# Performance work log

Hardware: AMD Instinct MI355X
Metric: run time of the kernel (lower is better)

## Reference

```python
import jax, jax.numpy as jnp
import numpy as np

C_ENC = 64
H_FEAT = 96
W_FEAT = 96
B = 2
Q = 32768
HID = 256
IN_DIM = C_ENC * 9 + 2 + 2  # 580
EPS_SHIFT = 1e-6


def _unfold3x3(feat):
    # F.unfold(feat, 3, padding=1).view(B, C*9, H, W)
    Bf, C, H, W = feat.shape
    p = jnp.pad(feat, ((0, 0), (0, 0), (1, 1), (1, 1)))
    shifts = [p[:, :, ki:ki + H, kj:kj + W] for ki in range(3) for kj in range(3)]
    return jnp.stack(shifts, axis=2).reshape(Bf, C * 9, H, W)


def _nearest_idx(g, size):
    # torch grid_sample nearest, align_corners=False: unnormalize then nearbyint
    ix = ((g + 1.0) * size - 1.0) * 0.5
    return jnp.clip(jnp.round(ix).astype(jnp.int32), 0, size - 1)


def _mlp(x, W0, b0, W1, b1, W2, b2, W3, b3, W4, b4):
    h = jax.nn.relu(x @ W0 + b0)
    h = jax.nn.relu(h @ W1 + b1)
    h = jax.nn.relu(h @ W2 + b2)
    h = jax.nn.relu(h @ W3 + b3)
    return h @ W4 + b4


def setup_inputs() -> dict:
    key = jax.random.key(0)
    ks = jax.random.split(key, 8)
    feat = jax.random.normal(ks[0], (B, C_ENC, H_FEAT, W_FEAT), jnp.float32)
    coord = jax.random.uniform(ks[1], (B, Q, 2), jnp.float32, -1.0, 1.0)
    # cell size for a ~181x181 HR grid: 2/181
    cell = jnp.full((B, Q, 2), 2.0 / 181.0, jnp.float32)
    s0 = 1.0 / np.sqrt(IN_DIM)
    sh = 1.0 / np.sqrt(HID)
    W0 = jax.random.normal(ks[2], (IN_DIM, HID), jnp.float32) * s0
    W1 = jax.random.normal(ks[3], (HID, HID), jnp.float32) * sh
    W2 = jax.random.normal(ks[4], (HID, HID), jnp.float32) * sh
    W3 = jax.random.normal(ks[5], (HID, HID), jnp.float32) * sh
    W4 = jax.random.normal(ks[6], (HID, 1), jnp.float32) * sh
    z = lambda n: jnp.zeros((n,), jnp.float32)
    return {"feat": feat, "coord": coord, "cell": cell,
            "W0": W0, "b0": z(HID), "W1": W1, "b1": z(HID),
            "W2": W2, "b2": z(HID), "W3": W3, "b3": z(HID),
            "W4": W4, "b4": z(1)}


def reference(feat, coord, cell, W0, b0, W1, b1, W2, b2, W3, b3, W4, b4):
    Bf, C, H, W = feat.shape
    feat_u = _unfold3x3(feat)                     # (B, C*9, H, W)
    feat_flat = feat_u.reshape(Bf, C * 9, H * W)  # (B, C9, HW)
    rx = 1.0 / H  # 2 / H / 2
    ry = 1.0 / W
    lo, hi = -1.0 + 1e-6, 1.0 - 1e-6
    rel_cell = cell * jnp.array([H, W], jnp.float32)  # (B,Q,2)

    preds, areas = [], []
    for vx in (-1.0, 1.0):
        for vy in (-1.0, 1.0):
            c0 = jnp.clip(coord[..., 0] + vx * rx + EPS_SHIFT, lo, hi)
            c1 = jnp.clip(coord[..., 1] + vy * ry + EPS_SHIFT, lo, hi)
            iy = _nearest_idx(c0, H)   # (B,Q) index into H dim
            ix = _nearest_idx(c1, W)
            lin = iy * W + ix
            q_feat = jnp.take_along_axis(feat_flat, lin[:, None, :], axis=2)
            q_feat = q_feat.transpose(0, 2, 1)  # (B,Q,C9)
            # pixel-center coords (= gathered make_coord grid)
            qc0 = (iy.astype(jnp.float32) + 0.5) * (2.0 / H) - 1.0
            qc1 = (ix.astype(jnp.float32) + 0.5) * (2.0 / W) - 1.0
            rel0 = (coord[..., 0] - qc0) * H
            rel1 = (coord[..., 1] - qc1) * W
            inp = jnp.concatenate(
                [q_feat, rel0[..., None], rel1[..., None], rel_cell], axis=-1)
            pred = _mlp(inp.reshape(Bf * inp.shape[1], -1),
                        W0, b0, W1, b1, W2, b2, W3, b3, W4, b4)
            preds.append(pred.reshape(Bf, -1, 1))
            areas.append(jnp.abs(rel0 * rel1) + 1e-9)

    tot_area = areas[0] + areas[1] + areas[2] + areas[3]
    # local-ensemble diagonal swap of areas
    areas = [areas[3], areas[2], areas[1], areas[0]]
    ret = jnp.zeros_like(preds[0])
    for pred, area in zip(preds, areas):
        ret = ret + pred * (area / tot_area)[..., None]
    return ret
```

## Files before the change

### kernel.cpp

```cpp
#include <hip/hip_runtime.h>
#include <hip/hip_bf16.h>

typedef __attribute__((ext_vector_type(8))) short bf16x8;
typedef __attribute__((ext_vector_type(4))) float f32x4;

#define NKT1 19

__device__ inline ushort f2bf(float f) {
    union { float f; unsigned u; } x; x.f = f;
    unsigned u = x.u;
    u += 0x7fffu + ((u >> 16) & 1u);
    return (ushort)(u >> 16);
}

__global__ void prep_feat_k(const float* __restrict__ feat, ushort* __restrict__ featT) {
    int idx = blockIdx.x * 256 + threadIdx.x;
    if (idx >= 2 * 96 * 96 * 64) return;
    int c = idx & 63;
    int rest = idx >> 6;
    int x = rest % 96; rest /= 96;
    int y = rest % 96;
    int b = rest / 96;
    featT[idx] = f2bf(feat[((b * 64 + c) * 96 + y) * 96 + x]);
}

__global__ void prep_w_k(const float* __restrict__ W, ushort* __restrict__ Wp,
                         int NT, int NKT, int Nstride, int mode) {
    int idx = blockIdx.x * 256 + threadIdx.x;
    if (idx >= NT * NKT * 64) return;
    int lane = idx & 63;
    int kt = (idx >> 6) % NKT;
    int nt = idx / (64 * NKT);
    int n = nt * 16 + (lane & 15);
    int kbase = kt * 32 + (lane >> 4) * 8;
    ushort o[8];
    #pragma unroll
    for (int i = 0; i < 8; ++i) {
        int k = kbase + i;
        float v = 0.0f;
        if (mode == 0) {
            if (k < 576) { int tap = k >> 6, c = k & 63; v = W[(c * 9 + tap) * Nstride + n]; }
            else if (k < 580) v = W[k * Nstride + n];
        } else if (mode == 1) {
            v = W[k * Nstride + n];
        } else {
            v = (n == 0) ? W[k] : 0.0f;
        }
        o[i] = f2bf(v);
    }
    *reinterpret_cast<uint4*>(Wp + (size_t)idx * 8) = *reinterpret_cast<const uint4*>(o);
}

template<int NKT>
__device__ inline void run_layer(const ushort* __restrict__ Wp,
                                 const float* __restrict__ bias,
                                 const ushort* A_lds, int lane, int w,
                                 f32x4 (&acc)[4][4]) {
    float bv[4];
    #pragma unroll
    for (int ct = 0; ct < 4; ++ct) bv[ct] = bias[(w * 4 + ct) * 16 + (lane & 15)];
    #pragma unroll
    for (int rt = 0; rt < 4; ++rt)
        #pragma unroll
        for (int ct = 0; ct < 4; ++ct) {
            acc[rt][ct][0] = bv[ct]; acc[rt][ct][1] = bv[ct];
            acc[rt][ct][2] = bv[ct]; acc[rt][ct][3] = bv[ct];
        }
    const int swl = lane ^ ((lane >> 3) & 3);
    for (int kt = 0; kt < NKT; ++kt) {
        bf16x8 a[4], b[4];
        #pragma unroll
        for (int rt = 0; rt < 4; ++rt)
            a[rt] = *reinterpret_cast<const bf16x8*>(A_lds + ((rt * NKT1 + kt) * 64 + swl) * 8);
        #pragma unroll
        for (int ct = 0; ct < 4; ++ct)
            b[ct] = *reinterpret_cast<const bf16x8*>(Wp + (((size_t)(w * 4 + ct) * NKT + kt) * 64 + lane) * 8);
        #pragma unroll
        for (int rt = 0; rt < 4; ++rt)
            #pragma unroll
            for (int ct = 0; ct < 4; ++ct)
                acc[rt][ct] = __builtin_amdgcn_mfma_f32_16x16x32_bf16(a[rt], b[ct], acc[rt][ct], 0, 0, 0);
    }
}

__device__ inline void store_acts(const f32x4 (&acc)[4][4], ushort* A_lds, int lane, int w) {
    #pragma unroll
    for (int rt = 0; rt < 4; ++rt)
        #pragma unroll
        for (int ct = 0; ct < 4; ++ct) {
            int col = (w * 4 + ct) * 16 + (lane & 15);
            int kt = col >> 5;
            int chk = (col & 31) >> 3;
            #pragma unroll
            for (int j = 0; j < 4; ++j) {
                int rowm = ((lane >> 4) << 2) + j;
                int slot = rowm + (chk << 4);
                int sw = slot ^ ((slot >> 3) & 3);
                A_lds[((rt * NKT1 + kt) * 64 + sw) * 8 + (col & 7)] =
                    f2bf(fmaxf(acc[rt][ct][j], 0.0f));
            }
        }
}

__global__ __launch_bounds__(256, 2) void liif_main(
    const float* __restrict__ coord, const float* __restrict__ cell,
    const ushort* __restrict__ featT,
    const ushort* __restrict__ W0p, const ushort* __restrict__ W1p,
    const ushort* __restrict__ W2p, const ushort* __restrict__ W3p,
    const ushort* __restrict__ W4p,
    const float* __restrict__ b0, const float* __restrict__ b1,
    const float* __restrict__ b2, const float* __restrict__ b3,
    const float* __restrict__ b4, float* __restrict__ out)
{
    __shared__ ushort A_lds[4 * NKT1 * 64 * 8];
    __shared__ float pred_lds[64];
    __shared__ float area_lds[64];

    const int t = threadIdx.x;
    const int lane = t & 63;
    const int w = t >> 6;

    {
        const int r = t >> 2, sub = t & 3;
        const int qi = r >> 2, s = r & 3;
        const int gq = blockIdx.x * 16 + qi;
        const int b = gq >> 15;
        const float vx = (s & 2) ? 1.0f : -1.0f;
        const float vy = (s & 1) ? 1.0f : -1.0f;
        const float rxf = (float)(1.0 / 96.0);
        const float lo = (float)(-1.0 + 1e-6);
        const float hi = (float)(1.0 - 1e-6);
        float c0 = coord[gq * 2 + 0], c1 = coord[gq * 2 + 1];
        float cl0 = cell[gq * 2 + 0], cl1 = cell[gq * 2 + 1];
        float sc0 = fminf(fmaxf(__fadd_rn(__fadd_rn(c0, vx * rxf), 1e-6f), lo), hi);
        float sc1 = fminf(fmaxf(__fadd_rn(__fadd_rn(c1, vy * rxf), 1e-6f), lo), hi);
        float fy = __fmul_rn(__fadd_rn(__fmul_rn(__fadd_rn(sc0, 1.0f), 96.0f), -1.0f), 0.5f);
        float fx = __fmul_rn(__fadd_rn(__fmul_rn(__fadd_rn(sc1, 1.0f), 96.0f), -1.0f), 0.5f);
        int iy = (int)rintf(fy); iy = iy < 0 ? 0 : (iy > 95 ? 95 : iy);
        int ix = (int)rintf(fx); ix = ix < 0 ? 0 : (ix > 95 ? 95 : ix);
        float qc0 = (iy + 0.5f) * (float)(2.0 / 96.0) - 1.0f;
        float qc1 = (ix + 0.5f) * (float)(2.0 / 96.0) - 1.0f;
        float rel0 = (c0 - qc0) * 96.0f;
        float rel1 = (c1 - qc1) * 96.0f;
        if (sub == 0) area_lds[r] = fabsf(rel0 * rel1) + 1e-9f;

        const int rt = r >> 4;
        const int slot = (r & 15) + (sub << 4);
        const int sw = slot ^ ((slot >> 3) & 3);
        const ushort* fb = featT + (size_t)b * 96 * 96 * 64;
        #pragma unroll
        for (int i = 0; i < 18; ++i) {
            int j = (i << 2) + sub;
            int tap = j >> 3;
            int cc = (j & 7) << 3;
            int yy = iy + (tap / 3) - 1;
            int xx = ix + (tap % 3) - 1;
            uint4 val = make_uint4(0, 0, 0, 0);
            if (yy >= 0 && yy < 96 && xx >= 0 && xx < 96)
                val = *reinterpret_cast<const uint4*>(fb + ((yy * 96 + xx) * 64 + cc));
            *reinterpret_cast<uint4*>(&A_lds[((rt * NKT1 + i) * 64 + sw) * 8]) = val;
        }
        {
            ushort ex[8] = {0, 0, 0, 0, 0, 0, 0, 0};
            if (sub == 0) {
                ex[0] = f2bf(rel0); ex[1] = f2bf(rel1);
                ex[2] = f2bf(cl0 * 96.0f); ex[3] = f2bf(cl1 * 96.0f);
            }
            *reinterpret_cast<uint4*>(&A_lds[((rt * NKT1 + 18) * 64 + sw) * 8]) =
                *reinterpret_cast<const uint4*>(ex);
        }
    }
    __syncthreads();

    f32x4 acc[4][4];
    run_layer<NKT1>(W0p, b0, A_lds, lane, w, acc);
    __syncthreads();
    store_acts(acc, A_lds, lane, w);
    __syncthreads();
    run_layer<8>(W1p, b1, A_lds, lane, w, acc);
    __syncthreads();
    store_acts(acc, A_lds, lane, w);
    __syncthreads();
    run_layer<8>(W2p, b2, A_lds, lane, w, acc);
    __syncthreads();
    store_acts(acc, A_lds, lane, w);
    __syncthreads();
    run_layer<8>(W3p, b3, A_lds, lane, w, acc);
    __syncthreads();
    store_acts(acc, A_lds, lane, w);
    __syncthreads();

    if (w == 0) {
        float b4v = b4[0];
        f32x4 a5[4];
        #pragma unroll
        for (int rt = 0; rt < 4; ++rt) { a5[rt][0] = b4v; a5[rt][1] = b4v; a5[rt][2] = b4v; a5[rt][3] = b4v; }
        const int swl = lane ^ ((lane >> 3) & 3);
        for (int kt = 0; kt < 8; ++kt) {
            bf16x8 bb = *reinterpret_cast<const bf16x8*>(W4p + ((size_t)kt * 64 + lane) * 8);
            #pragma unroll
            for (int rt = 0; rt < 4; ++rt) {
                bf16x8 aa = *reinterpret_cast<const bf16x8*>(A_lds + ((rt * NKT1 + kt) * 64 + swl) * 8);
                a5[rt] = __builtin_amdgcn_mfma_f32_16x16x32_bf16(aa, bb, a5[rt], 0, 0, 0);
            }
        }
        if ((lane & 15) == 0) {
            #pragma unroll
            for (int rt = 0; rt < 4; ++rt)
                #pragma unroll
                for (int j = 0; j < 4; ++j)
                    pred_lds[rt * 16 + ((lane >> 4) << 2) + j] = a5[rt][j];
        }
    }
    __syncthreads();

    if (t < 16) {
        int gq = blockIdx.x * 16 + t;
        float p0 = pred_lds[t * 4 + 0], p1 = pred_lds[t * 4 + 1];
        float p2 = pred_lds[t * 4 + 2], p3 = pred_lds[t * 4 + 3];
        float a0 = area_lds[t * 4 + 0], a1 = area_lds[t * 4 + 1];
        float a2 = area_lds[t * 4 + 2], a3 = area_lds[t * 4 + 3];
        float tot = a0 + a1 + a2 + a3;
        out[gq] = (p0 * a3 + p1 * a2 + p2 * a1 + p3 * a0) / tot;
    }
}

extern "C" void kernel_launch(void* const* d_in, const int* in_sizes, int n_in,
                              void* d_out, int out_size, void* d_ws, size_t ws_size,
                              hipStream_t stream) {
    const float* feat  = (const float*)d_in[0];
    const float* coord = (const float*)d_in[1];
    const float* cell  = (const float*)d_in[2];
    const float* W0 = (const float*)d_in[3];
    const float* b0 = (const float*)d_in[4];
    const float* W1 = (const float*)d_in[5];
    const float* b1 = (const float*)d_in[6];
    const float* W2 = (const float*)d_in[7];
    const float* b2 = (const float*)d_in[8];
    const float* W3 = (const float*)d_in[9];
    const float* b3 = (const float*)d_in[10];
    const float* W4 = (const float*)d_in[11];
    const float* b4 = (const float*)d_in[12];
    float* out = (float*)d_out;

    ushort* featT = (ushort*)d_ws;
    ushort* W0p = featT + 1179648;
    ushort* W1p = W0p + 155648;
    ushort* W2p = W1p + 65536;
    ushort* W3p = W2p + 65536;
    ushort* W4p = W3p + 65536;

    prep_feat_k<<<4608, 256, 0, stream>>>(feat, featT);
    prep_w_k<<<76, 256, 0, stream>>>(W0, W0p, 16, 19, 256, 0);
    prep_w_k<<<32, 256, 0, stream>>>(W1, W1p, 16, 8, 256, 1);
    prep_w_k<<<32, 256, 0, stream>>>(W2, W2p, 16, 8, 256, 1);
    prep_w_k<<<32, 256, 0, stream>>>(W3, W3p, 16, 8, 256, 1);
    prep_w_k<<<2, 256, 0, stream>>>(W4, W4p, 1, 8, 1, 2);
    liif_main<<<4096, 256, 0, stream>>>(coord, cell, featT, W0p, W1p, W2p, W3p, W4p,
                                        b0, b1, b2, b3, b4, out);
}
```

Baseline: 217.2 us.

## Use 512-thread blocks with 128-row tiles and chunked layer-0 K staging

The main kernel now runs 8 waves per block over 32 queries (128 rows), with each wave computing 2 column tiles across all 8 row tiles instead of 4x4. Layer 0's 19 K-steps are staged through LDS in chunks of 5 with a barrier per chunk. This shrinks the LDS buffer so more blocks fit per CU, and halves per-row weight traffic per block. The cost is more barriers and less A-fragment reuse per wave (each A load feeds only 2 MFMAs). The final projection is also split across all waves.

```diff
diff --git a/kernel.cpp b/kernel.cpp
--- a/kernel.cpp
+++ b/kernel.cpp
@@ -3,8 +3,6 @@
 
 typedef __attribute__((ext_vector_type(8))) short bf16x8;
 typedef __attribute__((ext_vector_type(4))) float f32x4;
-
-#define NKT1 19
 
 __device__ inline ushort f2bf(float f) {
     union { float f; unsigned u; } x; x.f = f;
@@ -51,58 +49,7 @@
     *reinterpret_cast<uint4*>(Wp + (size_t)idx * 8) = *reinterpret_cast<const uint4*>(o);
 }
 
-template<int NKT>
-__device__ inline void run_layer(const ushort* __restrict__ Wp,
-                                 const float* __restrict__ bias,
-                                 const ushort* A_lds, int lane, int w,
-                                 f32x4 (&acc)[4][4]) {
-    float bv[4];
-    #pragma unroll
-    for (int ct = 0; ct < 4; ++ct) bv[ct] = bias[(w * 4 + ct) * 16 + (lane & 15)];
-    #pragma unroll
-    for (int rt = 0; rt < 4; ++rt)
-        #pragma unroll
-        for (int ct = 0; ct < 4; ++ct) {
-            acc[rt][ct][0] = bv[ct]; acc[rt][ct][1] = bv[ct];
-            acc[rt][ct][2] = bv[ct]; acc[rt][ct][3] = bv[ct];
-        }
-    const int swl = lane ^ ((lane >> 3) & 3);
-    for (int kt = 0; kt < NKT; ++kt) {
-        bf16x8 a[4], b[4];
-        #pragma unroll
-        for (int rt = 0; rt < 4; ++rt)
-            a[rt] = *reinterpret_cast<const bf16x8*>(A_lds + ((rt * NKT1 + kt) * 64 + swl) * 8);
-        #pragma unroll
-        for (int ct = 0; ct < 4; ++ct)
-            b[ct] = *reinterpret_cast<const bf16x8*>(Wp + (((size_t)(w * 4 + ct) * NKT + kt) * 64 + lane) * 8);
-        #pragma unroll
-        for (int rt = 0; rt < 4; ++rt)
-            #pragma unroll
-            for (int ct = 0; ct < 4; ++ct)
-                acc[rt][ct] = __builtin_amdgcn_mfma_f32_16x16x32_bf16(a[rt], b[ct], acc[rt][ct], 0, 0, 0);
-    }
-}
-
-__device__ inline void store_acts(const f32x4 (&acc)[4][4], ushort* A_lds, int lane, int w) {
-    #pragma unroll
-    for (int rt = 0; rt < 4; ++rt)
-        #pragma unroll
-        for (int ct = 0; ct < 4; ++ct) {
-            int col = (w * 4 + ct) * 16 + (lane & 15);
-            int kt = col >> 5;
-            int chk = (col & 31) >> 3;
-            #pragma unroll
-            for (int j = 0; j < 4; ++j) {
-                int rowm = ((lane >> 4) << 2) + j;
-                int slot = rowm + (chk << 4);
-                int sw = slot ^ ((slot >> 3) & 3);
-                A_lds[((rt * NKT1 + kt) * 64 + sw) * 8 + (col & 7)] =
-                    f2bf(fmaxf(acc[rt][ct][j], 0.0f));
-            }
-        }
-}
-
-__global__ __launch_bounds__(256, 2) void liif_main(
+__global__ __launch_bounds__(512, 4) void liif_main(
     const float* __restrict__ coord, const float* __restrict__ cell,
     const ushort* __restrict__ featT,
     const ushort* __restrict__ W0p, const ushort* __restrict__ W1p,
@@ -112,19 +59,22 @@
     const float* __restrict__ b2, const float* __restrict__ b3,
     const float* __restrict__ b4, float* __restrict__ out)
 {
-    __shared__ ushort A_lds[4 * NKT1 * 64 * 8];
-    __shared__ float pred_lds[64];
-    __shared__ float area_lds[64];
+    __shared__ ushort buf[8 * 8 * 64 * 8];
+    __shared__ float pred_lds[128];
+    __shared__ float area_lds[128];
 
     const int t = threadIdx.x;
     const int lane = t & 63;
     const int w = t >> 6;
-
+    const int swl = lane ^ ((lane >> 3) & 3);
+
+    const int r = t >> 2, sub = t & 3;
+    const int qi = r >> 2, s = r & 3;
+    const int gq = blockIdx.x * 32 + qi;
+    const int bidx = gq >> 15;
+    int iy, ix;
+    float rel0, rel1, rc0, rc1;
     {
-        const int r = t >> 2, sub = t & 3;
-        const int qi = r >> 2, s = r & 3;
-        const int gq = blockIdx.x * 16 + qi;
-        const int b = gq >> 15;
         const float vx = (s & 2) ? 1.0f : -1.0f;
         const float vy = (s & 1) ? 1.0f : -1.0f;
         const float rxf = (float)(1.0 / 96.0);
@@ -136,92 +86,155 @@
         float sc1 = fminf(fmaxf(__fadd_rn(__fadd_rn(c1, vy * rxf), 1e-6f), lo), hi);
         float fy = __fmul_rn(__fadd_rn(__fmul_rn(__fadd_rn(sc0, 1.0f), 96.0f), -1.0f), 0.5f);
         float fx = __fmul_rn(__fadd_rn(__fmul_rn(__fadd_rn(sc1, 1.0f), 96.0f), -1.0f), 0.5f);
-        int iy = (int)rintf(fy); iy = iy < 0 ? 0 : (iy > 95 ? 95 : iy);
-        int ix = (int)rintf(fx); ix = ix < 0 ? 0 : (ix > 95 ? 95 : ix);
+        iy = (int)rintf(fy); iy = iy < 0 ? 0 : (iy > 95 ? 95 : iy);
+        ix = (int)rintf(fx); ix = ix < 0 ? 0 : (ix > 95 ? 95 : ix);
         float qc0 = (iy + 0.5f) * (float)(2.0 / 96.0) - 1.0f;
         float qc1 = (ix + 0.5f) * (float)(2.0 / 96.0) - 1.0f;
-        float rel0 = (c0 - qc0) * 96.0f;
-        float rel1 = (c1 - qc1) * 96.0f;
+        rel0 = (c0 - qc0) * 96.0f;
+        rel1 = (c1 - qc1) * 96.0f;
+        rc0 = cl0 * 96.0f; rc1 = cl1 * 96.0f;
         if (sub == 0) area_lds[r] = fabsf(rel0 * rel1) + 1e-9f;
-
-        const int rt = r >> 4;
-        const int slot = (r & 15) + (sub << 4);
-        const int sw = slot ^ ((slot >> 3) & 3);
-        const ushort* fb = featT + (size_t)b * 96 * 96 * 64;
-        #pragma unroll
-        for (int i = 0; i < 18; ++i) {
-            int j = (i << 2) + sub;
-            int tap = j >> 3;
-            int cc = (j & 7) << 3;
-            int yy = iy + (tap / 3) - 1;
-            int xx = ix + (tap % 3) - 1;
+    }
+    const int g_rt = r >> 4;
+    const int g_slot = (r & 15) + (sub << 4);
+    const int g_sw = g_slot ^ ((g_slot >> 3) & 3);
+    const ushort* fb = featT + (size_t)bidx * 96 * 96 * 64;
+
+    f32x4 acc[8][2];
+    {
+        float bv0 = b0[(w * 2 + 0) * 16 + (lane & 15)];
+        float bv1 = b0[(w * 2 + 1) * 16 + (lane & 15)];
+        #pragma unroll
+        for (int rt = 0; rt < 8; ++rt) {
+            acc[rt][0][0] = bv0; acc[rt][0][1] = bv0; acc[rt][0][2] = bv0; acc[rt][0][3] = bv0;
+            acc[rt][1][0] = bv1; acc[rt][1][1] = bv1; acc[rt][1][2] = bv1; acc[rt][1][3] = bv1;
+        }
+    }
+    #pragma unroll 1
+    for (int p = 0; p < 4; ++p) {
+        const int nkt = (p == 3) ? 4 : 5;
+        #pragma unroll
+        for (int i = 0; i < 5; ++i) {
+            int kt = p * 5 + i;
+            if (i >= nkt) break;
             uint4 val = make_uint4(0, 0, 0, 0);
-            if (yy >= 0 && yy < 96 && xx >= 0 && xx < 96)
-                val = *reinterpret_cast<const uint4*>(fb + ((yy * 96 + xx) * 64 + cc));
-            *reinterpret_cast<uint4*>(&A_lds[((rt * NKT1 + i) * 64 + sw) * 8]) = val;
-        }
-        {
-            ushort ex[8] = {0, 0, 0, 0, 0, 0, 0, 0};
-            if (sub == 0) {
+            if (kt < 18) {
+                int j = (kt << 2) + sub;
+                int tap = j >> 3;
+                int cc = (j & 7) << 3;
+                int yy = iy + (tap / 3) - 1;
+                int xx = ix + (tap % 3) - 1;
+                if (yy >= 0 && yy < 96 && xx >= 0 && xx < 96)
+                    val = *reinterpret_cast<const uint4*>(fb + ((yy * 96 + xx) * 64 + cc));
+            } else if (sub == 0) {
+                ushort ex[8] = {0, 0, 0, 0, 0, 0, 0, 0};
                 ex[0] = f2bf(rel0); ex[1] = f2bf(rel1);
-                ex[2] = f2bf(cl0 * 96.0f); ex[3] = f2bf(cl1 * 96.0f);
-            }
-            *reinterpret_cast<uint4*>(&A_lds[((rt * NKT1 + 18) * 64 + sw) * 8]) =
-                *reinterpret_cast<const uint4*>(ex);
-        }
-    }
+                ex[2] = f2bf(rc0);  ex[3] = f2bf(rc1);
+                val = *reinterpret_cast<const uint4*>(ex);
+            }
+            *reinterpret_cast<uint4*>(&buf[((g_rt * 5 + i) * 64 + g_sw) * 8]) = val;
+        }
+        __syncthreads();
+        #pragma unroll 1
+        for (int i = 0; i < nkt; ++i) {
+            int kt = p * 5 + i;
+            bf16x8 b0f = *reinterpret_cast<const bf16x8*>(W0p + (((size_t)(w * 2 + 0) * 19 + kt) * 64 + lane) * 8);
+            bf16x8 b1f = *reinterpret_cast<const bf16x8*>(W0p + (((size_t)(w * 2 + 1) * 19 + kt) * 64 + lane) * 8);
+            #pragma unroll
+            for (int rt = 0; rt < 8; ++rt) {
+                bf16x8 a = *reinterpret_cast<const bf16x8*>(buf + ((rt * 5 + i) * 64 + swl) * 8);
+                acc[rt][0] = __builtin_amdgcn_mfma_f32_16x16x32_bf16(a, b0f, acc[rt][0], 0, 0, 0);
+                acc[rt][1] = __builtin_amdgcn_mfma_f32_16x16x32_bf16(a, b1f, acc[rt][1], 0, 0, 0);
+            }
+        }
+        __syncthreads();
+    }
+
+    #pragma unroll 1
+    for (int layer = 0; layer < 3; ++layer) {
+        #pragma unroll
+        for (int rt = 0; rt < 8; ++rt)
+            #pragma unroll
+            for (int ct = 0; ct < 2; ++ct) {
+                int col = (w * 2 + ct) * 16 + (lane & 15);
+                int kt = col >> 5;
+                int chk = (col & 31) >> 3;
+                #pragma unroll
+                for (int j = 0; j < 4; ++j) {
+                    int rowm = ((lane >> 4) << 2) + j;
+                    int slot = rowm + (chk << 4);
+                    int sw = slot ^ ((slot >> 3) & 3);
+                    buf[((rt * 8 + kt) * 64 + sw) * 8 + (col & 7)] =
+                        f2bf(fmaxf(acc[rt][ct][j], 0.0f));
+                }
+            }
+        __syncthreads();
+        const ushort* Wp = (layer == 0) ? W1p : (layer == 1) ? W2p : W3p;
+        const float* bias = (layer == 0) ? b1 : (layer == 1) ? b2 : b3;
+        float bv0 = bias[(w * 2 + 0) * 16 + (lane & 15)];
+        float bv1 = bias[(w * 2 + 1) * 16 + (lane & 15)];
+        #pragma unroll
+        for (int rt = 0; rt < 8; ++rt) {
+            acc[rt][0][0] = bv0; acc[rt][0][1] = bv0; acc[rt][0][2] = bv0; acc[rt][0][3] = bv0;
+            acc[rt][1][0] = bv1; acc[rt][1][1] = bv1; acc[rt][1][2] = bv1; acc[rt][1][3] = bv1;
+        }
+        #pragma unroll 1
+        for (int kt = 0; kt < 8; ++kt) {
+            bf16x8 b0f = *reinterpret_cast<const bf16x8*>(Wp + (((size_t)(w * 2 + 0) * 8 + kt) * 64 + lane) * 8);
+            bf16x8 b1f = *reinterpret_cast<const bf16x8*>(Wp + (((size_t)(w * 2 + 1) * 8 + kt) * 64 + lane) * 8);
+            #pragma unroll
+            for (int rt = 0; rt < 8; ++rt) {
+                bf16x8 a = *reinterpret_cast<const bf16x8*>(buf + ((rt * 8 + kt) * 64 + swl) * 8);
+                acc[rt][0] = __builtin_amdgcn_mfma_f32_16x16x32_bf16(a, b0f, acc[rt][0], 0, 0, 0);
+                acc[rt][1] = __builtin_amdgcn_mfma_f32_16x16x32_bf16(a, b1f, acc[rt][1], 0, 0, 0);
+            }
+        }
+        __syncthreads();
+    }
+    #pragma unroll
+    for (int rt = 0; rt < 8; ++rt)
+        #pragma unroll
+        for (int ct = 0; ct < 2; ++ct) {
+            int col = (w * 2 + ct) * 16 + (lane & 15);
+            int kt = col >> 5;
+            int chk = (col & 31) >> 3;
+            #pragma unroll
+            for (int j = 0; j < 4; ++j) {
+                int rowm = ((lane >> 4) << 2) + j;
+                int slot = rowm + (chk << 4);
+                int sw = slot ^ ((slot >> 3) & 3);
+                buf[((rt * 8 + kt) * 64 + sw) * 8 + (col & 7)] =
+                    f2bf(fmaxf(acc[rt][ct][j], 0.0f));
+            }
+        }
     __syncthreads();
 
-    f32x4 acc[4][4];
-    run_layer<NKT1>(W0p, b0, A_lds, lane, w, acc);
-    __syncthreads();
-    store_acts(acc, A_lds, lane, w);
-    __syncthreads();
-    run_layer<8>(W1p, b1, A_lds, lane, w, acc);
-    __syncthreads();
-    store_acts(acc, A_lds, lane, w);
-    __syncthreads();
-    run_layer<8>(W2p, b2, A_lds, lane, w, acc);
-    __syncthreads();
-    store_acts(acc, A_lds, lane, w);
-    __syncthreads();
-    run_layer<8>(W3p, b3, A_lds, lane, w, acc);
-    __syncthreads();
-    store_acts(acc, A_lds, lane, w);
-    __syncthreads();
-
-    if (w == 0) {
+    {
         float b4v = b4[0];
-        f32x4 a5[4];
-        #pragma unroll
-        for (int rt = 0; rt < 4; ++rt) { a5[rt][0] = b4v; a5[rt][1] = b4v; a5[rt][2] = b4v; a5[rt][3] = b4v; }
-        const int swl = lane ^ ((lane >> 3) & 3);
+        f32x4 a5;
+        a5[0] = b4v; a5[1] = b4v; a5[2] = b4v; a5[3] = b4v;
+        #pragma unroll
         for (int kt = 0; kt < 8; ++kt) {
             bf16x8 bb = *reinterpret_cast<const bf16x8*>(W4p + ((size_t)kt * 64 + lane) * 8);
-            #pragma unroll
-            for (int rt = 0; rt < 4; ++rt) {
-                bf16x8 aa = *reinterpret_cast<const bf16x8*>(A_lds + ((rt * NKT1 + kt) * 64 + swl) * 8);
-                a5[rt] = __builtin_amdgcn_mfma_f32_16x16x32_bf16(aa, bb, a5[rt], 0, 0, 0);
-            }
+            bf16x8 aa = *reinterpret_cast<const bf16x8*>(buf + ((w * 8 + kt) * 64 + swl) * 8);
+            a5 = __builtin_amdgcn_mfma_f32_16x16x32_bf16(aa, bb, a5, 0, 0, 0);
         }
         if ((lane & 15) == 0) {
             #pragma unroll
-            for (int rt = 0; rt < 4; ++rt)
-                #pragma unroll
-                for (int j = 0; j < 4; ++j)
-                    pred_lds[rt * 16 + ((lane >> 4) << 2) + j] = a5[rt][j];
+            for (int j = 0; j < 4; ++j)
+                pred_lds[w * 16 + ((lane >> 4) << 2) + j] = a5[j];
         }
     }
     __syncthreads();
 
-    if (t < 16) {
-        int gq = blockIdx.x * 16 + t;
+    if (t < 32) {
+        int oq = blockIdx.x * 32 + t;
         float p0 = pred_lds[t * 4 + 0], p1 = pred_lds[t * 4 + 1];
         float p2 = pred_lds[t * 4 + 2], p3 = pred_lds[t * 4 + 3];
         float a0 = area_lds[t * 4 + 0], a1 = area_lds[t * 4 + 1];
         float a2 = area_lds[t * 4 + 2], a3 = area_lds[t * 4 + 3];
         float tot = a0 + a1 + a2 + a3;
-        out[gq] = (p0 * a3 + p1 * a2 + p2 * a1 + p3 * a0) / tot;
+        out[oq] = (p0 * a3 + p1 * a2 + p2 * a1 + p3 * a0) / tot;
     }
 }
 
@@ -256,6 +269,6 @@
     prep_w_k<<<32, 256, 0, stream>>>(W2, W2p, 16, 8, 256, 1);
     prep_w_k<<<32, 256, 0, stream>>>(W3, W3p, 16, 8, 256, 1);
     prep_w_k<<<2, 256, 0, stream>>>(W4, W4p, 1, 8, 1, 2);
-    liif_main<<<4096, 256, 0, stream>>>(coord, cell, featT, W0p, W1p, W2p, W3p, W4p,
+    liif_main<<<2048, 512, 0, stream>>>(coord, cell, featT, W0p, W1p, W2p, W3p, W4p,
                                         b0, b1, b2, b3, b4, out);
 }
```

Measured after the change: 290.3 us. 33.6% more time.
